# Optimization experiments

Measured on AMD Instinct MI355X. Metric: run time of the kernel, lower is better.

## Reference

```python
import jax, jax.numpy as jnp
import numpy as np

HEADS = 8
DIM_HEAD = 64


def setup_inputs() -> dict:
    key = jax.random.key(0)
    ks = jax.random.split(key, 5)
    dim = 512
    dim_inner = HEADS * DIM_HEAD
    return {
        "fmap": jax.random.normal(ks[0], (8, dim, 32, 32), dtype=jnp.float32),
        "gamma": jnp.ones((dim,), dtype=jnp.float32),
        "wq": jax.random.normal(ks[1], (dim_inner, dim), dtype=jnp.float32) * 0.05,
        "wv": jax.random.normal(ks[2], (dim_inner, dim), dtype=jnp.float32) * 0.05,
        "null_kv": jax.random.normal(ks[3], (2, HEADS, DIM_HEAD), dtype=jnp.float32),
        "wo": jax.random.normal(ks[4], (dim, dim_inner), dtype=jnp.float32) * 0.05,
    }


def reference(fmap, gamma, wq, wv, null_kv, wo):
    b, c, H, W = fmap.shape
    h, d = HEADS, DIM_HEAD
    n = H * W
    scale = d ** (-0.5)

    # ChannelRMSNorm: F.normalize over channel dim * sqrt(dim) * gamma
    l2 = jnp.sqrt(jnp.sum(fmap * fmap, axis=1, keepdims=True))
    x = fmap / jnp.maximum(l2, 1e-12) * (c ** 0.5) * gamma[None, :, None, None]

    # 1x1 convs as channel matmuls -> [b, h, n, d]
    def proj(w):
        t = jnp.einsum('bcxy,oc->boxy', x, w)          # [b, h*d, H, W]
        return t.reshape(b, h, d, n).transpose(0, 1, 3, 2)  # [b, h, n, d]

    q = proj(wq)
    v = proj(wv)
    k = q  # dot_product=False -> to_k is None, k = q

    # prepend null kv token
    nk = jnp.broadcast_to(null_kv[0][None, :, None, :], (b, h, 1, d))
    nv = jnp.broadcast_to(null_kv[1][None, :, None, :], (b, h, 1, d))
    k = jnp.concatenate([nk, k], axis=2)  # [b, h, n+1, d]
    v = jnp.concatenate([nv, v], axis=2)

    # negative squared L2 distance score: -(|q|^2 + |k|^2 - 2 q.k)
    q_sq = jnp.sum(q * q, axis=-1)  # [b, h, n]
    k_sq = jnp.sum(k * k, axis=-1)  # [b, h, n+1]
    qk = jnp.einsum('bhid,bhjd->bhij', q, k)
    sim = -(q_sq[..., :, None] + k_sq[..., None, :] - 2.0 * qk) * scale

    attn = jax.nn.softmax(sim, axis=-1)
    out = jnp.einsum('bhij,bhjd->bhid', attn, v)  # [b, h, n, d]

    out = out.transpose(0, 1, 3, 2).reshape(b, h * d, H, W)
    return jnp.einsum('boxy,co->bcxy', out, wo)
```

## Files before the change

### kernel.cpp

```cpp
#include <hip/hip_runtime.h>
#include <hip/hip_bf16.h>

#define DEV static __device__ __forceinline__

typedef __bf16 bf16x8 __attribute__((ext_vector_type(8)));
typedef float f32x4 __attribute__((ext_vector_type(4)));
typedef float f32x16 __attribute__((ext_vector_type(16)));
typedef unsigned u32x4 __attribute__((ext_vector_type(4)));
typedef unsigned short u16x8 __attribute__((ext_vector_type(8)));
typedef unsigned short u16x4 __attribute__((ext_vector_type(4)));

DEV unsigned short f2bf(float f) {
  unsigned u = __builtin_bit_cast(unsigned, f);
  u += 0x7fffu + ((u >> 16) & 1u);
  return (unsigned short)(u >> 16);
}
DEV float bf2f(unsigned short s) {
  return __builtin_bit_cast(float, (unsigned)s << 16);
}
DEV f32x4 mfma16(bf16x8 a, bf16x8 b, f32x4 c) {
  return __builtin_amdgcn_mfma_f32_16x16x32_bf16(a, b, c, 0, 0, 0);
}
DEV f32x16 mfma32(bf16x8 a, bf16x8 b, f32x16 c) {
  return __builtin_amdgcn_mfma_f32_32x32x16_bf16(a, b, c, 0, 0, 0);
}
DEV bf16x8 ld8(const unsigned short* p) {
  return __builtin_bit_cast(bf16x8, *(const u16x8*)p);
}

__global__ __launch_bounds__(256) void prep_k(const float* __restrict__ wq,
                                              const float* __restrict__ wv,
                                              const float* __restrict__ wo,
                                              const float* __restrict__ fmap,
                                              unsigned short* __restrict__ wqb,
                                              unsigned short* __restrict__ wvb,
                                              unsigned short* __restrict__ wob,
                                              float* __restrict__ rn) {
  __shared__ float red[4][64];
  int bid = blockIdx.x, tid = threadIdx.x;
  if (bid < 384) {
    int g = bid >> 7;
    int i = (bid & 127) * 256 + tid;
    const float* src = (g == 0) ? wq : (g == 1) ? wv : wo;
    unsigned short* dst = (g == 0) ? wqb : (g == 1) ? wvb : wob;
    const float4* s = (const float4*)src;
    float4 a = s[i * 2], b = s[i * 2 + 1];
    u16x8 o;
    o[0] = f2bf(a.x); o[1] = f2bf(a.y); o[2] = f2bf(a.z); o[3] = f2bf(a.w);
    o[4] = f2bf(b.x); o[5] = f2bf(b.y); o[6] = f2bf(b.z); o[7] = f2bf(b.w);
    ((u16x8*)dst)[i] = o;
  } else {
    int bb = bid - 384;
    int x = bb & 15, b = bb >> 4;
    int nl = tid & 63, cq = tid >> 6;
    int n = x * 64 + nl;
    const float* p = fmap + ((size_t)(b * 512 + cq * 128)) * 1024 + n;
    float s = 0.f;
#pragma unroll 8
    for (int i = 0; i < 128; ++i) { float v = p[i * 1024]; s += v * v; }
    red[cq][nl] = s;
    __syncthreads();
    if (tid < 64) {
      float t = red[0][tid] + red[1][tid] + red[2][tid] + red[3][tid];
      rn[b * 1024 + x * 64 + tid] = 22.62741699796952f / fmaxf(sqrtf(t), 1e-12f);
    }
  }
}

__global__ __launch_bounds__(256) void tnorm_k(const float* __restrict__ fmap,
                                               const float* __restrict__ gamma,
                                               const float* __restrict__ rn,
                                               unsigned short* __restrict__ xt) {
  int b = blockIdx.z, c0 = blockIdx.y * 64, n0 = blockIdx.x * 64;
  __shared__ float t[64][65];
  __shared__ float rnl[64], gl[64];
  int tid = threadIdx.x;
  int tx = tid & 63, ty = tid >> 6;
#pragma unroll
  for (int i = 0; i < 16; ++i) {
    int r = ty * 16 + i;
    t[r][tx] = fmap[((size_t)(b * 512 + c0 + r)) * 1024 + n0 + tx];
  }
  if (tid < 64) rnl[tid] = rn[b * 1024 + n0 + tid];
  else if (tid < 128) gl[tid - 64] = gamma[c0 + tid - 64];
  __syncthreads();
#pragma unroll
  for (int half = 0; half < 2; ++half) {
    int nl = (tid >> 3) + half * 32;
    int cb = (tid & 7) * 8;
    float s = rnl[nl];
    u16x8 o;
#pragma unroll
    for (int e = 0; e < 8; ++e) o[e] = f2bf(t[cb + e][nl] * s * gl[cb + e]);
    *(u16x8*)(xt + ((size_t)(b * 1024 + n0 + nl)) * 512 + c0 + cb) = o;
  }
}

__global__ __launch_bounds__(256) void gemm_qv_k(const unsigned short* __restrict__ A,
                                                 const unsigned short* __restrict__ wqb,
                                                 const unsigned short* __restrict__ wvb,
                                                 const float* __restrict__ nkv,
                                                 unsigned short* __restrict__ QF,
                                                 unsigned short* __restrict__ VF,
                                                 float* __restrict__ qsqs,
                                                 float* __restrict__ p0g) {
  __shared__ unsigned short a_lds[128][72];
  __shared__ unsigned short b_lds[128][72];
  const unsigned short* Bt = blockIdx.z ? wvb : wqb;
  int tid = threadIdx.x, lane = tid & 63, wid = tid >> 6;
  int wr = wid >> 1, wc = wid & 1;
  int m0 = blockIdx.y * 128, n0 = blockIdx.x * 128;
  f32x4 acc[4][4] = {};
  for (int kt = 0; kt < 512; kt += 64) {
#pragma unroll
    for (int it = 0; it < 4; ++it) {
      int chunk = it * 256 + tid;
      int row = chunk >> 3, col = (chunk & 7) * 8;
      *(u16x8*)(&a_lds[row][col]) = *(const u16x8*)(A + (size_t)(m0 + row) * 512 + kt + col);
      *(u16x8*)(&b_lds[row][col]) = *(const u16x8*)(Bt + (size_t)(n0 + row) * 512 + kt + col);
    }
    __syncthreads();
#pragma unroll
    for (int ks = 0; ks < 2; ++ks) {
      bf16x8 af[4], bfr[4];
#pragma unroll
      for (int rt = 0; rt < 4; ++rt)
        af[rt] = __builtin_bit_cast(bf16x8,
            *(const u16x8*)(&a_lds[wr * 64 + rt * 16 + (lane & 15)][ks * 32 + (lane >> 4) * 8]));
#pragma unroll
      for (int ct = 0; ct < 4; ++ct)
        bfr[ct] = __builtin_bit_cast(bf16x8,
            *(const u16x8*)(&b_lds[wc * 64 + ct * 16 + (lane & 15)][ks * 32 + (lane >> 4) * 8]));
#pragma unroll
      for (int rt = 0; rt < 4; ++rt)
#pragma unroll
        for (int ct = 0; ct < 4; ++ct)
          acc[rt][ct] = mfma16(af[rt], bfr[ct], acc[rt][ct]);
    }
    __syncthreads();
  }
  if (blockIdx.z == 0) {
    const float COEF = 0.18033688011112042f;
    int head = blockIdx.x * 2 + wc;
    const float* nk = nkv + head * 64;
    float nk_own[4], nks = 0.f;
#pragma unroll
    for (int ct = 0; ct < 4; ++ct) {
      nk_own[ct] = nk[ct * 16 + (lane & 15)];
      nks += nk_own[ct] * nk_own[ct];
    }
    nks += __shfl_xor(nks, 1); nks += __shfl_xor(nks, 2);
    nks += __shfl_xor(nks, 4); nks += __shfl_xor(nks, 8);
#pragma unroll
    for (int rt = 0; rt < 4; ++rt)
#pragma unroll
      for (int r = 0; r < 4; ++r) {
        float qs = 0.f, dot = 0.f;
        unsigned short qr[4];
#pragma unroll
        for (int ct = 0; ct < 4; ++ct) {
          unsigned short us = f2bf(acc[rt][ct][r]);
          qr[ct] = us;
          float v = bf2f(us);
          qs += v * v;
          dot += v * nk_own[ct];
        }
        int n = m0 + wr * 64 + rt * 16 + (lane >> 4) * 4 + r;
        int bb = n >> 10, nl = n & 1023;
        int bh = bb * 8 + head;
        size_t fidx = (size_t)(bh * 32 + (nl >> 5)) * 2048 + (nl & 31) * 16 + (lane & 15);
#pragma unroll
        for (int ct = 0; ct < 4; ++ct) QF[fidx + ct * 512] = qr[ct];
        qs += __shfl_xor(qs, 1); qs += __shfl_xor(qs, 2);
        qs += __shfl_xor(qs, 4); qs += __shfl_xor(qs, 8);
        dot += __shfl_xor(dot, 1); dot += __shfl_xor(dot, 2);
        dot += __shfl_xor(dot, 4); dot += __shfl_xor(dot, 8);
        if ((lane & 15) == 0) {
          qsqs[bh * 1024 + nl] = qs * COEF;
          p0g[bh * 1024 + nl] = __builtin_amdgcn_exp2f((2.f * dot - nks) * COEF);
        }
      }
  } else {
#pragma unroll
    for (int rt = 0; rt < 4; ++rt)
#pragma unroll
      for (int ct = 0; ct < 4; ++ct) {
        int nb = m0 + wr * 64 + rt * 16 + (lane >> 4) * 4;
        int o = n0 + wc * 64 + ct * 16 + (lane & 15);
        int b = nb >> 10, j = nb & 1023;
        int h = o >> 6, d = o & 63;
        int bh = b * 8 + h;
        size_t idx = (size_t)(bh * 32 + (j >> 5)) * 2048 + ((j >> 4) & 1) * 1024 + (d >> 5) * 512 +
                     (d & 31) * 16 + (j & 15);
        u16x4 pk;
#pragma unroll
        for (int r = 0; r < 4; ++r) pk[r] = f2bf(acc[rt][ct][r]);
        *(u16x4*)(VF + idx) = pk;
      }
  }
}

__global__ __launch_bounds__(256) void gemm_o_k(const unsigned short* __restrict__ A,
                                                const unsigned short* __restrict__ Bt,
                                                float* __restrict__ Cp) {
  __shared__ unsigned short a_lds[128][72];
  __shared__ unsigned short b_lds[128][72];
  int tid = threadIdx.x, lane = tid & 63, wid = tid >> 6;
  int wr = wid >> 1, wc = wid & 1;
  int m0 = blockIdx.y * 128, n0 = blockIdx.x * 128;
  f32x4 acc[4][4] = {};
  for (int kt = 0; kt < 512; kt += 64) {
#pragma unroll
    for (int it = 0; it < 4; ++it) {
      int chunk = it * 256 + tid;
      int row = chunk >> 3, col = (chunk & 7) * 8;
      *(u16x8*)(&a_lds[row][col]) = *(const u16x8*)(A + (size_t)(m0 + row) * 512 + kt + col);
      *(u16x8*)(&b_lds[row][col]) = *(const u16x8*)(Bt + (size_t)(n0 + row) * 512 + kt + col);
    }
    __syncthreads();
#pragma unroll
    for (int ks = 0; ks < 2; ++ks) {
      bf16x8 af[4], bfr[4];
#pragma unroll
      for (int rt = 0; rt < 4; ++rt)
        af[rt] = __builtin_bit_cast(bf16x8,
            *(const u16x8*)(&a_lds[wr * 64 + rt * 16 + (lane & 15)][ks * 32 + (lane >> 4) * 8]));
#pragma unroll
      for (int ct = 0; ct < 4; ++ct)
        bfr[ct] = __builtin_bit_cast(bf16x8,
            *(const u16x8*)(&b_lds[wc * 64 + ct * 16 + (lane & 15)][ks * 32 + (lane >> 4) * 8]));
#pragma unroll
      for (int rt = 0; rt < 4; ++rt)
#pragma unroll
        for (int ct = 0; ct < 4; ++ct)
          acc[rt][ct] = mfma16(af[rt], bfr[ct], acc[rt][ct]);
    }
    __syncthreads();
  }
  int bb = n0 >> 10;
#pragma unroll
  for (int rt = 0; rt < 4; ++rt)
#pragma unroll
    for (int ct = 0; ct < 4; ++ct)
#pragma unroll
      for (int r = 0; r < 4; ++r) {
        int row = m0 + wr * 64 + rt * 16 + (lane >> 4) * 4 + r;
        int col = (n0 & 1023) + wc * 64 + ct * 16 + (lane & 15);
        Cp[((size_t)(bb * 512 + row)) * 1024 + col] = acc[rt][ct][r];
      }
}

__global__ __launch_bounds__(512) void attn_k(const unsigned short* __restrict__ QF,
                                              const unsigned short* __restrict__ VF,
                                              const float* __restrict__ qsqs,
                                              const float* __restrict__ p0g,
                                              const float* __restrict__ nkv,
                                              unsigned short* __restrict__ att) {
  const float C2 = 0.36067376022224085f;
  int bid = blockIdx.x;
  int s0 = bid >> 3;
  int bh = ((bid & 7) << 3) | (s0 & 7);
  int qt = s0 >> 3;
  int b = bh >> 3, h = bh & 7;
  int n0 = qt * 128;
  int tid = threadIdx.x, lane = tid & 63, wid = tid >> 6;
  int wq = wid & 3, jg = wid >> 2;
  int l31 = lane & 31, hi = lane >> 5;

  __shared__ float ob_l[32][4][64];
  __shared__ float dsb[4][32];
  __shared__ float p0_l[128];
  __shared__ float nv_l[64];
  __shared__ float dn_l[4][32];

  if (tid < 128) p0_l[tid] = p0g[bh * 1024 + n0 + tid];
  else if (tid < 192) nv_l[tid - 128] = nkv[512 + h * 64 + (tid - 128)];
  __syncthreads();

  bf16x8 qf[4];
  const unsigned short* qfp = QF + (size_t)(bh * 32 + qt * 4 + wq) * 2048 + l31 * 16 + hi * 8;
#pragma unroll
  for (int ks = 0; ks < 4; ++ks)
    qf[ks] = ld8(qfp + ks * 512);

  f32x16 oacc[2];
#pragma unroll
  for (int dh = 0; dh < 2; ++dh)
#pragma unroll
    for (int r = 0; r < 16; ++r) {
      int row = (r & 3) + 8 * (r >> 2) + 4 * hi;
      oacc[dh][r] = (jg == 0) ? p0_l[wq * 32 + row] * nv_l[dh * 32 + l31] : 0.f;
    }

  f32x4 dsum4 = {0.f, 0.f, 0.f, 0.f};
  const unsigned short* kbase = QF + (size_t)bh * 65536 + l31 * 16 + hi * 8;
  const unsigned short* vbase = VF + (size_t)bh * 65536 + l31 * 16 + hi * 8;
  const float* ksb = qsqs + bh * 1024 + 4 * hi;

  bf16x8 kfA[4], kfB[4], vfA[2][2], vfB[2][2];
  f32x4 ksqA[4], ksqB[4];

#define LOADT(S, JT)                                                        \
  {                                                                         \
    const unsigned short* kp_ = kbase + (JT) * 2048;                        \
    kf##S[0] = ld8(kp_);        kf##S[1] = ld8(kp_ + 512);                  \
    kf##S[2] = ld8(kp_ + 1024); kf##S[3] = ld8(kp_ + 1536);                 \
    const unsigned short* vp_ = vbase + (JT) * 2048;                        \
    vf##S[0][0] = ld8(vp_);        vf##S[0][1] = ld8(vp_ + 1024);           \
    vf##S[1][0] = ld8(vp_ + 512);  vf##S[1][1] = ld8(vp_ + 1536);           \
    const float* kq_ = ksb + (JT) * 32;                                     \
    ksq##S[0] = *(const f32x4*)(kq_);      ksq##S[1] = *(const f32x4*)(kq_ + 8);  \
    ksq##S[2] = *(const f32x4*)(kq_ + 16); ksq##S[3] = *(const f32x4*)(kq_ + 24); \
  }

#define COMPT(S)                                                            \
  {                                                                         \
    f32x16 sacc = {};                                                       \
    __builtin_amdgcn_s_setprio(1);                                          \
    sacc = mfma32(kf##S[0], qf[0], sacc);                                   \
    sacc = mfma32(kf##S[1], qf[1], sacc);                                   \
    sacc = mfma32(kf##S[2], qf[2], sacc);                                   \
    sacc = mfma32(kf##S[3], qf[3], sacc);                                   \
    __builtin_amdgcn_s_setprio(0);                                          \
    float p[16];                                                            \
    _Pragma("unroll")                                                       \
    for (int r = 0; r < 16; ++r) {                                          \
      p[r] = __builtin_amdgcn_exp2f(sacc[r] * C2 - ksq##S[r >> 2][r & 3]);  \
      dsum4[r & 3] += p[r];                                                 \
    }                                                                       \
    unsigned w[4][2];                                                       \
    _Pragma("unroll")                                                       \
    for (int m = 0; m < 4; ++m) {                                           \
      asm("v_cvt_pk_bf16_f32 %0, %1, %2" : "=v"(w[m][0]) : "v"(p[4 * m]), "v"(p[4 * m + 1]));     \
      asm("v_cvt_pk_bf16_f32 %0, %1, %2" : "=v"(w[m][1]) : "v"(p[4 * m + 2]), "v"(p[4 * m + 3])); \
    }                                                                       \
    __builtin_amdgcn_s_setprio(1);                                          \
    _Pragma("unroll")                                                       \
    for (int sj = 0; sj < 2; ++sj) {                                        \
      unsigned a0 = w[2 * sj][0], b0 = w[2 * sj + 1][0];                    \
      unsigned a1 = w[2 * sj][1], b1 = w[2 * sj + 1][1];                    \
      asm("v_permlane32_swap_b32 %0, %1" : "+v"(a0), "+v"(b0));             \
      asm("v_permlane32_swap_b32 %0, %1" : "+v"(a1), "+v"(b1));             \
      u32x4 pw; pw[0] = a0; pw[1] = a1; pw[2] = b0; pw[3] = b1;             \
      bf16x8 pa = __builtin_bit_cast(bf16x8, pw);                           \
      oacc[0] = mfma32(pa, vf##S[0][sj], oacc[0]);                          \
      oacc[1] = mfma32(pa, vf##S[1][sj], oacc[1]);                          \
    }                                                                       \
    __builtin_amdgcn_s_setprio(0);                                          \
  }

  int jb = jg * 16;
  LOADT(A, jb)
#pragma unroll 1
  for (int s = 0; s < 7; ++s) {
    LOADT(B, jb + 2 * s + 1)
    COMPT(A)
    LOADT(A, jb + 2 * s + 2)
    COMPT(B)
  }
  LOADT(B, jb + 15)
  COMPT(A)
  COMPT(B)

  float dsum = (dsum4[0] + dsum4[1]) + (dsum4[2] + dsum4[3]);
  dsum += __shfl_xor(dsum, 32);

  if (jg == 1) {
#pragma unroll
    for (int dh = 0; dh < 2; ++dh)
#pragma unroll
      for (int r = 0; r < 16; ++r)
        ob_l[dh * 16 + r][wq][lane] = oacc[dh][r];
    if (hi == 0) dsb[wq][l31] = dsum;
  }
  __syncthreads();
  if (jg == 0) {
#pragma unroll
    for (int dh = 0; dh < 2; ++dh)
#pragma unroll
      for (int r = 0; r < 16; ++r)
        oacc[dh][r] += ob_l[dh * 16 + r][wq][lane];
    dsum += dsb[wq][l31] + p0_l[wq * 32 + l31];
    float rden = 1.0f / dsum;
    if (hi == 0) dn_l[wq][l31] = rden;
  }
  __syncthreads();

  if (jg == 0) {
#pragma unroll
    for (int dh = 0; dh < 2; ++dh)
#pragma unroll
      for (int r = 0; r < 16; ++r) {
        int row = (r & 3) + 8 * (r >> 2) + 4 * hi;
        float o = oacc[dh][r] * dn_l[wq][row];
        att[((size_t)(b * 1024 + n0 + wq * 32 + row)) * 512 + h * 64 + dh * 32 + l31] = f2bf(o);
      }
  }
}

extern "C" void kernel_launch(void* const* d_in, const int* in_sizes, int n_in,
                              void* d_out, int out_size, void* d_ws, size_t ws_size,
                              hipStream_t stream) {
  const float* fmap = (const float*)d_in[0];
  const float* gamma = (const float*)d_in[1];
  const float* wq = (const float*)d_in[2];
  const float* wv = (const float*)d_in[3];
  const float* nkv = (const float*)d_in[4];
  const float* wo = (const float*)d_in[5];
  float* out = (float*)d_out;

  const size_t M4 = (size_t)8192 * 512;
  unsigned short* x_t = (unsigned short*)d_ws;
  unsigned short* QF  = x_t + M4;
  unsigned short* VF  = QF + M4;
  unsigned short* att = VF + M4;
  unsigned short* wqb = att + M4;
  unsigned short* wvb = wqb + (size_t)512 * 512;
  unsigned short* wob = wvb + (size_t)512 * 512;
  float* rn   = (float*)(wob + (size_t)512 * 512);
  float* qsqs = rn + 8192;
  float* p0g  = qsqs + 65536;

  prep_k<<<512, 256, 0, stream>>>(wq, wv, wo, fmap, wqb, wvb, wob, rn);
  tnorm_k<<<dim3(16, 8, 8), 256, 0, stream>>>(fmap, gamma, rn, x_t);
  gemm_qv_k<<<dim3(4, 64, 2), 256, 0, stream>>>(x_t, wqb, wvb, nkv, QF, VF, qsqs, p0g);
  attn_k<<<512, 512, 0, stream>>>(QF, VF, qsqs, p0g, nkv, att);
  gemm_o_k<<<dim3(64, 4), 256, 0, stream>>>(wob, att, out);
}
```

Baseline: 76.93 us.

## Fuse norm into prep kernel, use direct global-to-LDS loads with XOR swizzle

Merges the RMS-norm reduction and the transpose/normalize kernel into one prep kernel, so the per-pixel norm no longer round-trips through global memory and one launch is removed. Both GEMMs switch from register-staged LDS fills to global_load_lds direct loads into XOR-swizzled unpadded LDS tiles, which cuts VGPR traffic while avoiding bank conflicts. The output GEMM uses smaller 64x128 tiles (512 blocks) with a remapped block order for better CU coverage and L2 locality. The fused prep kernel has fewer blocks (256 working on the norm) that each loop over all channels, which risks lower parallelism in that stage.

Measured after the change: 70.05 us. -8.9%, faster.

```diff
diff --git a/kernel.cpp b/kernel.cpp
--- a/kernel.cpp
+++ b/kernel.cpp
@@ -27,72 +27,75 @@
 DEV bf16x8 ld8(const unsigned short* p) {
   return __builtin_bit_cast(bf16x8, *(const u16x8*)p);
 }
-
-__global__ __launch_bounds__(256) void prep_k(const float* __restrict__ wq,
+DEV void gload16(const unsigned short* g, unsigned short* l) {
+  auto* g1 = reinterpret_cast<const __attribute__((address_space(1))) unsigned int*>(
+      reinterpret_cast<uintptr_t>(g));
+  auto* l3 = reinterpret_cast<__attribute__((address_space(3))) unsigned int*>(
+      reinterpret_cast<uintptr_t>(l));
+  __builtin_amdgcn_global_load_lds(g1, l3, 16, 0, 0);
+}
+
+__global__ __launch_bounds__(256) void prep_k(const float* __restrict__ fmap,
+                                              const float* __restrict__ gamma,
+                                              const float* __restrict__ wq,
                                               const float* __restrict__ wv,
                                               const float* __restrict__ wo,
-                                              const float* __restrict__ fmap,
+                                              unsigned short* __restrict__ xt,
                                               unsigned short* __restrict__ wqb,
                                               unsigned short* __restrict__ wvb,
-                                              unsigned short* __restrict__ wob,
-                                              float* __restrict__ rn) {
-  __shared__ float red[4][64];
+                                              unsigned short* __restrict__ wob) {
   int bid = blockIdx.x, tid = threadIdx.x;
-  if (bid < 384) {
-    int g = bid >> 7;
-    int i = (bid & 127) * 256 + tid;
+  if (bid >= 256) {
+    int t4 = bid - 256;
+    int g = t4 >> 5;
     const float* src = (g == 0) ? wq : (g == 1) ? wv : wo;
     unsigned short* dst = (g == 0) ? wqb : (g == 1) ? wvb : wob;
+    int base = (t4 & 31) * 1024 + tid;
     const float4* s = (const float4*)src;
-    float4 a = s[i * 2], b = s[i * 2 + 1];
+#pragma unroll
+    for (int i = 0; i < 4; ++i) {
+      int idx = base + i * 256;
+      float4 a = s[idx * 2], b = s[idx * 2 + 1];
+      u16x8 o;
+      o[0] = f2bf(a.x); o[1] = f2bf(a.y); o[2] = f2bf(a.z); o[3] = f2bf(a.w);
+      o[4] = f2bf(b.x); o[5] = f2bf(b.y); o[6] = f2bf(b.z); o[7] = f2bf(b.w);
+      ((u16x8*)dst)[idx] = o;
+    }
+    return;
+  }
+  __shared__ float red[8][32];
+  __shared__ float rn_l[32];
+  __shared__ float gl[512];
+  __shared__ float t[64][33];
+  int b = bid >> 5, n0 = (bid & 31) * 32;
+  gl[tid] = gamma[tid];
+  gl[tid + 256] = gamma[tid + 256];
+  int n_l = tid & 31, cg = tid >> 5;
+  const float* p = fmap + ((size_t)(b * 512 + cg * 64)) * 1024 + n0 + n_l;
+  float s = 0.f;
+#pragma unroll 16
+  for (int i = 0; i < 64; ++i) { float v = p[i * 1024]; s += v * v; }
+  red[cg][n_l] = s;
+  __syncthreads();
+  if (tid < 32) {
+    float ts = 0.f;
+#pragma unroll
+    for (int k = 0; k < 8; ++k) ts += red[k][tid];
+    rn_l[tid] = 22.62741699796952f / fmaxf(sqrtf(ts), 1e-12f);
+  }
+  __syncthreads();
+  int nn = tid >> 3, cc = tid & 7;
+  for (int c0 = 0; c0 < 512; c0 += 64) {
+#pragma unroll
+    for (int i = 0; i < 8; ++i)
+      t[cg * 8 + i][n_l] = fmap[((size_t)(b * 512 + c0 + cg * 8 + i)) * 1024 + n0 + n_l];
+    __syncthreads();
+    float sc = rn_l[nn];
     u16x8 o;
-    o[0] = f2bf(a.x); o[1] = f2bf(a.y); o[2] = f2bf(a.z); o[3] = f2bf(a.w);
-    o[4] = f2bf(b.x); o[5] = f2bf(b.y); o[6] = f2bf(b.z); o[7] = f2bf(b.w);
-    ((u16x8*)dst)[i] = o;
-  } else {
-    int bb = bid - 384;
-    int x = bb & 15, b = bb >> 4;
-    int nl = tid & 63, cq = tid >> 6;
-    int n = x * 64 + nl;
-    const float* p = fmap + ((size_t)(b * 512 + cq * 128)) * 1024 + n;
-    float s = 0.f;
-#pragma unroll 8
-    for (int i = 0; i < 128; ++i) { float v = p[i * 1024]; s += v * v; }
-    red[cq][nl] = s;
-    __syncthreads();
-    if (tid < 64) {
-      float t = red[0][tid] + red[1][tid] + red[2][tid] + red[3][tid];
-      rn[b * 1024 + x * 64 + tid] = 22.62741699796952f / fmaxf(sqrtf(t), 1e-12f);
-    }
-  }
-}
-
-__global__ __launch_bounds__(256) void tnorm_k(const float* __restrict__ fmap,
-                                               const float* __restrict__ gamma,
-                                               const float* __restrict__ rn,
-                                               unsigned short* __restrict__ xt) {
-  int b = blockIdx.z, c0 = blockIdx.y * 64, n0 = blockIdx.x * 64;
-  __shared__ float t[64][65];
-  __shared__ float rnl[64], gl[64];
-  int tid = threadIdx.x;
-  int tx = tid & 63, ty = tid >> 6;
-#pragma unroll
-  for (int i = 0; i < 16; ++i) {
-    int r = ty * 16 + i;
-    t[r][tx] = fmap[((size_t)(b * 512 + c0 + r)) * 1024 + n0 + tx];
-  }
-  if (tid < 64) rnl[tid] = rn[b * 1024 + n0 + tid];
-  else if (tid < 128) gl[tid - 64] = gamma[c0 + tid - 64];
-  __syncthreads();
-#pragma unroll
-  for (int half = 0; half < 2; ++half) {
-    int nl = (tid >> 3) + half * 32;
-    int cb = (tid & 7) * 8;
-    float s = rnl[nl];
-    u16x8 o;
-#pragma unroll
-    for (int e = 0; e < 8; ++e) o[e] = f2bf(t[cb + e][nl] * s * gl[cb + e]);
-    *(u16x8*)(xt + ((size_t)(b * 1024 + n0 + nl)) * 512 + c0 + cb) = o;
+#pragma unroll
+    for (int e = 0; e < 8; ++e) o[e] = f2bf(t[cc * 8 + e][nn] * sc * gl[c0 + cc * 8 + e]);
+    *(u16x8*)(xt + ((size_t)(b * 1024 + n0 + nn)) * 512 + c0 + cc * 8) = o;
+    __syncthreads();
   }
 }
 
@@ -104,33 +107,34 @@
                                                  unsigned short* __restrict__ VF,
                                                  float* __restrict__ qsqs,
                                                  float* __restrict__ p0g) {
-  __shared__ unsigned short a_lds[128][72];
-  __shared__ unsigned short b_lds[128][72];
+  __shared__ unsigned short a_lds[128 * 64];
+  __shared__ unsigned short b_lds[128 * 64];
   const unsigned short* Bt = blockIdx.z ? wvb : wqb;
   int tid = threadIdx.x, lane = tid & 63, wid = tid >> 6;
   int wr = wid >> 1, wc = wid & 1;
   int m0 = blockIdx.y * 128, n0 = blockIdx.x * 128;
+  int srow = (lane >> 3);
+  int scol = ((lane & 7) ^ ((lane >> 3) & 7)) * 8;
   f32x4 acc[4][4] = {};
   for (int kt = 0; kt < 512; kt += 64) {
 #pragma unroll
-    for (int it = 0; it < 4; ++it) {
-      int chunk = it * 256 + tid;
-      int row = chunk >> 3, col = (chunk & 7) * 8;
-      *(u16x8*)(&a_lds[row][col]) = *(const u16x8*)(A + (size_t)(m0 + row) * 512 + kt + col);
-      *(u16x8*)(&b_lds[row][col]) = *(const u16x8*)(Bt + (size_t)(n0 + row) * 512 + kt + col);
+    for (int i = 0; i < 4; ++i) {
+      int il = wid * 4 + i;
+      gload16(A + (size_t)(m0 + il * 8 + srow) * 512 + kt + scol, &a_lds[il * 512]);
+      gload16(Bt + (size_t)(n0 + il * 8 + srow) * 512 + kt + scol, &b_lds[il * 512]);
     }
     __syncthreads();
 #pragma unroll
     for (int ks = 0; ks < 2; ++ks) {
+      int c = ks * 4 + (lane >> 4);
+      int cs = (c ^ (lane & 7)) * 8;
       bf16x8 af[4], bfr[4];
 #pragma unroll
       for (int rt = 0; rt < 4; ++rt)
-        af[rt] = __builtin_bit_cast(bf16x8,
-            *(const u16x8*)(&a_lds[wr * 64 + rt * 16 + (lane & 15)][ks * 32 + (lane >> 4) * 8]));
+        af[rt] = ld8(&a_lds[(wr * 64 + rt * 16 + (lane & 15)) * 64 + cs]);
 #pragma unroll
       for (int ct = 0; ct < 4; ++ct)
-        bfr[ct] = __builtin_bit_cast(bf16x8,
-            *(const u16x8*)(&b_lds[wc * 64 + ct * 16 + (lane & 15)][ks * 32 + (lane >> 4) * 8]));
+        bfr[ct] = ld8(&b_lds[(wc * 64 + ct * 16 + (lane & 15)) * 64 + cs]);
 #pragma unroll
       for (int rt = 0; rt < 4; ++rt)
 #pragma unroll
@@ -203,34 +207,42 @@
 __global__ __launch_bounds__(256) void gemm_o_k(const unsigned short* __restrict__ A,
                                                 const unsigned short* __restrict__ Bt,
                                                 float* __restrict__ Cp) {
-  __shared__ unsigned short a_lds[128][72];
-  __shared__ unsigned short b_lds[128][72];
+  __shared__ unsigned short a_lds[64 * 64];
+  __shared__ unsigned short b_lds[128 * 64];
+  int bid = blockIdx.x;
+  int y = (bid >> 3) & 7;
+  int x = (bid & 7) + ((bid >> 6) << 3);
+  int m0 = y * 64, n0 = x * 128;
   int tid = threadIdx.x, lane = tid & 63, wid = tid >> 6;
   int wr = wid >> 1, wc = wid & 1;
-  int m0 = blockIdx.y * 128, n0 = blockIdx.x * 128;
-  f32x4 acc[4][4] = {};
+  int srow = (lane >> 3);
+  int scol = ((lane & 7) ^ ((lane >> 3) & 7)) * 8;
+  f32x4 acc[2][4] = {};
   for (int kt = 0; kt < 512; kt += 64) {
 #pragma unroll
-    for (int it = 0; it < 4; ++it) {
-      int chunk = it * 256 + tid;
-      int row = chunk >> 3, col = (chunk & 7) * 8;
-      *(u16x8*)(&a_lds[row][col]) = *(const u16x8*)(A + (size_t)(m0 + row) * 512 + kt + col);
-      *(u16x8*)(&b_lds[row][col]) = *(const u16x8*)(Bt + (size_t)(n0 + row) * 512 + kt + col);
+    for (int i = 0; i < 2; ++i) {
+      int il = wid * 2 + i;
+      gload16(A + (size_t)(m0 + il * 8 + srow) * 512 + kt + scol, &a_lds[il * 512]);
+    }
+#pragma unroll
+    for (int i = 0; i < 4; ++i) {
+      int il = wid * 4 + i;
+      gload16(Bt + (size_t)(n0 + il * 8 + srow) * 512 + kt + scol, &b_lds[il * 512]);
     }
     __syncthreads();
 #pragma unroll
     for (int ks = 0; ks < 2; ++ks) {
-      bf16x8 af[4], bfr[4];
-#pragma unroll
-      for (int rt = 0; rt < 4; ++rt)
-        af[rt] = __builtin_bit_cast(bf16x8,
-            *(const u16x8*)(&a_lds[wr * 64 + rt * 16 + (lane & 15)][ks * 32 + (lane >> 4) * 8]));
+      int c = ks * 4 + (lane >> 4);
+      int cs = (c ^ (lane & 7)) * 8;
+      bf16x8 af[2], bfr[4];
+#pragma unroll
+      for (int rt = 0; rt < 2; ++rt)
+        af[rt] = ld8(&a_lds[(wr * 32 + rt * 16 + (lane & 15)) * 64 + cs]);
 #pragma unroll
       for (int ct = 0; ct < 4; ++ct)
-        bfr[ct] = __builtin_bit_cast(bf16x8,
-            *(const u16x8*)(&b_lds[wc * 64 + ct * 16 + (lane & 15)][ks * 32 + (lane >> 4) * 8]));
-#pragma unroll
-      for (int rt = 0; rt < 4; ++rt)
+        bfr[ct] = ld8(&b_lds[(wc * 64 + ct * 16 + (lane & 15)) * 64 + cs]);
+#pragma unroll
+      for (int rt = 0; rt < 2; ++rt)
 #pragma unroll
         for (int ct = 0; ct < 4; ++ct)
           acc[rt][ct] = mfma16(af[rt], bfr[ct], acc[rt][ct]);
@@ -239,12 +251,12 @@
   }
   int bb = n0 >> 10;
 #pragma unroll
-  for (int rt = 0; rt < 4; ++rt)
+  for (int rt = 0; rt < 2; ++rt)
 #pragma unroll
     for (int ct = 0; ct < 4; ++ct)
 #pragma unroll
       for (int r = 0; r < 4; ++r) {
-        int row = m0 + wr * 64 + rt * 16 + (lane >> 4) * 4 + r;
+        int row = m0 + wr * 32 + rt * 16 + (lane >> 4) * 4 + r;
         int col = (n0 & 1023) + wc * 64 + ct * 16 + (lane & 15);
         Cp[((size_t)(bb * 512 + row)) * 1024 + col] = acc[rt][ct][r];
       }
@@ -417,13 +429,11 @@
   unsigned short* wqb = att + M4;
   unsigned short* wvb = wqb + (size_t)512 * 512;
   unsigned short* wob = wvb + (size_t)512 * 512;
-  float* rn   = (float*)(wob + (size_t)512 * 512);
-  float* qsqs = rn + 8192;
+  float* qsqs = (float*)(wob + (size_t)512 * 512);
   float* p0g  = qsqs + 65536;
 
-  prep_k<<<512, 256, 0, stream>>>(wq, wv, wo, fmap, wqb, wvb, wob, rn);
-  tnorm_k<<<dim3(16, 8, 8), 256, 0, stream>>>(fmap, gamma, rn, x_t);
+  prep_k<<<352, 256, 0, stream>>>(fmap, gamma, wq, wv, wo, x_t, wqb, wvb, wob);
   gemm_qv_k<<<dim3(4, 64, 2), 256, 0, stream>>>(x_t, wqb, wvb, nkv, QF, VF, qsqs, p0g);
   attn_k<<<512, 512, 0, stream>>>(QF, VF, qsqs, p0g, nkv, att);
-  gemm_o_k<<<dim3(64, 4), 256, 0, stream>>>(wob, att, out);
-}
+  gemm_o_k<<<512, 256, 0, stream>>>(wob, att, out);
+}
```
